# Kernel optimization log

Hardware: AMD Instinct MI355X
Metric: run time of the kernel (lower is better)

The kernel has to match this reference:

```python
import jax, jax.numpy as jnp
import numpy as np

C = 32          # d_model / channels
D_STATE = 32
D_CONV = 4
EXPAND = 2
D_INNER = EXPAND * C          # 64
DT_RANK = (C + 15) // 16      # ceil(32/16) = 2
EPS = 1e-5


def _conv2d(x, w, b):
    # x: (B,C,H,W), w: (O,I,3,3), stride 1, padding 1 (torch Conv2d)
    y = jax.lax.conv_general_dilated(
        x, w, window_strides=(1, 1), padding=[(1, 1), (1, 1)],
        dimension_numbers=("NCHW", "OIHW", "NCHW"))
    return y + b[None, :, None, None]


def _silu(x):
    return x * jax.nn.sigmoid(x)


def _mamba(xs, in_proj_w, conv1d_w, conv1d_b, x_proj_w, dt_proj_w, dt_proj_b,
           A_log, Dp, out_proj_w):
    # xs: (B, L, C)
    xz = xs @ in_proj_w.T                       # (B, L, 2*D_INNER)
    xm, z = jnp.split(xz, 2, axis=-1)           # each (B, L, D_INNER)

    # causal depthwise conv1d along L (torch: padding=d_conv-1 then [..., :L])
    xc = xm.transpose(0, 2, 1)                  # (B, D_INNER, L)
    xc = jax.lax.conv_general_dilated(
        xc, conv1d_w, window_strides=(1,), padding=[(D_CONV - 1, 0)],
        dimension_numbers=("NCH", "OIH", "NCH"),
        feature_group_count=D_INNER)
    xm = _silu((xc + conv1d_b[None, :, None]).transpose(0, 2, 1))  # (B,L,D_INNER)

    x_dbl = xm @ x_proj_w.T                     # (B, L, DT_RANK + 2*D_STATE)
    dt = x_dbl[..., :DT_RANK]
    Bm = x_dbl[..., DT_RANK:DT_RANK + D_STATE]  # (B, L, N)
    Cm = x_dbl[..., DT_RANK + D_STATE:]         # (B, L, N)

    delta = jax.nn.softplus(dt @ dt_proj_w.T + dt_proj_b)  # (B, L, D_INNER)
    A = -jnp.exp(A_log)                                     # (D_INNER, N)

    deltaA = jnp.exp(delta[..., None] * A)                           # (B,L,D,N)
    deltaBx = delta[..., None] * Bm[:, :, None, :] * xm[..., None]   # (B,L,D,N)

    def combine(c1, c2):
        a1, b1 = c1
        a2, b2 = c2
        return a1 * a2, a2 * b1 + b2

    # parallel linear recurrence h_t = deltaA_t * h_{t-1} + deltaBx_t
    _, hstate = jax.lax.associative_scan(combine, (deltaA, deltaBx), axis=1)

    y = jnp.einsum("bldn,bln->bld", hstate, Cm) + xm * Dp
    y = y * _silu(z)
    return y @ out_proj_w.T                     # (B, L, C)


def setup_inputs() -> dict:
    key = jax.random.key(0)
    ks = jax.random.split(key, 16)
    s = 0.02
    inp = {
        "x": jax.random.normal(ks[0], (4, C, 64, 64), dtype=jnp.float32),
        "conv1_w": jax.random.normal(ks[1], (2 * C, C, 3, 3), jnp.float32) * s,
        "conv1_b": jnp.zeros((2 * C,), jnp.float32),
        "conv2_w": jax.random.normal(ks[2], (C, 2 * C, 3, 3), jnp.float32) * s,
        "conv2_b": jnp.zeros((C,), jnp.float32),
        "ln_g": jnp.ones((C,), jnp.float32),
        "ln_b": jnp.zeros((C,), jnp.float32),
        "in_proj_w": jax.random.normal(ks[3], (2 * D_INNER, C), jnp.float32) * s,
        "conv1d_w": jax.random.normal(ks[4], (D_INNER, 1, D_CONV), jnp.float32) * 0.1,
        "conv1d_b": jnp.zeros((D_INNER,), jnp.float32),
        "x_proj_w": jax.random.normal(ks[5], (DT_RANK + 2 * D_STATE, D_INNER), jnp.float32) * s,
        "dt_proj_w": jax.random.normal(ks[6], (D_INNER, DT_RANK), jnp.float32) * 0.1,
        "dt_proj_b": jax.random.normal(ks[7], (D_INNER,), jnp.float32) * 0.1 - 4.0,
        "A_log": jnp.log(jnp.tile(jnp.arange(1, D_STATE + 1, dtype=jnp.float32), (D_INNER, 1))),
        "Dp": jnp.ones((D_INNER,), jnp.float32),
        "out_proj_w": jax.random.normal(ks[8], (C, D_INNER), jnp.float32) * s,
        "smooth_w": jax.random.normal(ks[9], (C, C, 3, 3), jnp.float32) * s,
        "smooth_b": jnp.zeros((C,), jnp.float32),
    }
    return inp


def reference(x, conv1_w, conv1_b, conv2_w, conv2_b, ln_g, ln_b,
              in_proj_w, conv1d_w, conv1d_b, x_proj_w, dt_proj_w, dt_proj_b,
              A_log, Dp, out_proj_w, smooth_w, smooth_b):
    b, c, h, w = x.shape
    # convb residual
    t = jax.nn.relu(_conv2d(x, conv1_w, conv1_b))
    x = _conv2d(t, conv2_w, conv2_b) + x
    # reshape (b,c,h,w) -> (b, h*w, c) row-major (faithful to torch .reshape)
    xs = x.reshape(b, -1, c)
    # LayerNorm over last dim
    mu = jnp.mean(xs, axis=-1, keepdims=True)
    var = jnp.mean(jnp.square(xs - mu), axis=-1, keepdims=True)
    xs = (xs - mu) * jax.lax.rsqrt(var + EPS) * ln_g + ln_b
    # Mamba block
    y = _mamba(xs, in_proj_w, conv1d_w, conv1d_b, x_proj_w, dt_proj_w,
               dt_proj_b, A_log, Dp, out_proj_w)
    y = y.transpose(0, 2, 1).reshape(b, c, h, w)
    return _conv2d(y, smooth_w, smooth_b)
```

## Files before the change

### kernel.cpp

```cpp
#include <hip/hip_runtime.h>
#include <math.h>

#define SEQL 4096
#define L2E 1.44269504088896340736f

#if defined(__has_builtin)
#if __has_builtin(__builtin_amdgcn_exp2f)
#define FAST_EXP2(x) __builtin_amdgcn_exp2f(x)
#endif
#endif
#ifndef FAST_EXP2
#define FAST_EXP2(x) exp2f(x)
#endif

__device__ __forceinline__ float sigmoid_f(float x){ return 1.0f/(1.0f+expf(-x)); }

template<int CI, int CO, int COG, bool RELU, bool RES>
__global__ __launch_bounds__(256) void conv3x3_k(const float* __restrict__ in,
    const float* __restrict__ wgt, const float* __restrict__ bias,
    const float* __restrict__ res, float* __restrict__ out)
{
  constexpr int CIT = CI/4;
  __shared__ float tin[4][2][6][72];
  __shared__ float red[3][4][COG][66];
  const int tid  = threadIdx.x;
  const int lane = tid & 63;
  const int ty   = tid >> 6;
  const int tyu  = __builtin_amdgcn_readfirstlane(ty);
  const int h0   = blockIdx.x * 4;
  const int co0  = blockIdx.y * COG;
  const int b    = blockIdx.z;

  if (lane < 24){
    int cl = lane / 12, rem = lane % 12, r = rem >> 1, side = rem & 1;
    tin[ty][cl][r][side ? 68 : 3] = 0.0f;
  }

  float acc[4][COG];
  #pragma unroll
  for (int rr=0;rr<4;++rr)
    #pragma unroll
    for (int u=0;u<COG;++u) acc[rr][u] = 0.0f;

  const int ci0 = tyu*CIT;
  for (int cig = ci0; cig < ci0 + CIT; cig += 2){
    #pragma unroll
    for (int k=0;k<3;++k){
      int idx4 = lane + (k<<6);
      int row  = idx4 >> 4;
      int cl = row/6, r = row - cl*6;
      int w4 = (idx4 & 15) << 2;
      int h  = h0 - 1 + r;
      float4 v = make_float4(0.f,0.f,0.f,0.f);
      if (h>=0 && h<64)
        v = *(const float4*)(in + ((size_t)(b*CI+cig+cl)*64 + h)*64 + w4);
      *(float4*)&tin[ty][cl][r][4+w4] = v;
    }
    #pragma unroll
    for (int cl=0; cl<2; ++cl){
      float rv[6][3];
      #pragma unroll
      for (int r=0;r<6;++r)
        #pragma unroll
        for (int c=0;c<3;++c)
          rv[r][c] = tin[ty][cl][r][3+lane+c];
      #pragma unroll
      for (int u=0;u<COG;++u){
        const float* wp = wgt + ((size_t)(co0+u)*CI + cig + cl)*9;
        #pragma unroll
        for (int rr=0;rr<4;++rr)
          #pragma unroll
          for (int j=0;j<3;++j){
            acc[rr][u] = fmaf(rv[rr+j][0], wp[3*j+0], acc[rr][u]);
            acc[rr][u] = fmaf(rv[rr+j][1], wp[3*j+1], acc[rr][u]);
            acc[rr][u] = fmaf(rv[rr+j][2], wp[3*j+2], acc[rr][u]);
          }
      }
    }
  }
  if (ty > 0){
    #pragma unroll
    for (int rr=0;rr<4;++rr)
      #pragma unroll
      for (int u=0;u<COG;++u) red[ty-1][rr][u][lane] = acc[rr][u];
  }
  __syncthreads();
  if (ty == 0){
    #pragma unroll
    for (int rr=0;rr<4;++rr)
      #pragma unroll
      for (int u=0;u<COG;++u){
        float s = acc[rr][u] + red[0][rr][u][lane] + red[1][rr][u][lane]
                + red[2][rr][u][lane] + bias[co0+u];
        size_t ob = ((size_t)(b*CO+co0+u)*64 + h0+rr)*64 + lane;
        if constexpr (RES)  s += res[ob];
        if constexpr (RELU) s = fmaxf(s, 0.0f);
        out[ob] = s;
      }
  }
}

__global__ __launch_bounds__(1024, 4) void mamba_in_k(const float* __restrict__ x2,
    const float* __restrict__ g, const float* __restrict__ be,
    const float* __restrict__ Wip, const float* __restrict__ cw,
    const float* __restrict__ cb, const float* __restrict__ Wxp,
    const float* __restrict__ Wdt, const float* __restrict__ bdt,
    const float* __restrict__ A_log,
    float* __restrict__ xm2, float* __restrict__ szb, float* __restrict__ dlt,
    float* __restrict__ Bm, float* __restrict__ Cm,
    float* __restrict__ cA, float* __restrict__ cH)
{
  __shared__ __align__(16) float xn[68][37];
  __shared__ __align__(16) float xm[64][68];
  __shared__ __align__(16) float xtT[64][68];
  __shared__ __align__(16) float xd[64][67];
  float (*xbT)[68] = reinterpret_cast<float(*)[68]>(&xn[0][0]);
  const int tid = threadIdx.x, lane = tid & 63, ty = tid >> 6;
  const int tyu = __builtin_amdgcn_readfirstlane(ty);
  const int bi = blockIdx.x >> 6;
  const int l0 = (blockIdx.x & 63) << 6;

  {
    const int row = tid >> 3, sub = tid & 7;
    if (row < 67){
      const int tok = l0 - 3 + row;
      const int c0 = sub << 2;
      if (tok >= 0){
        float4 f = *(const float4*)(x2 + (size_t)bi*131072 + (size_t)tok*32 + c0);
        float s = (f.x+f.y)+(f.z+f.w);
        s += __shfl_xor(s,1); s += __shfl_xor(s,2); s += __shfl_xor(s,4);
        const float mu = s * 0.03125f;
        float dx=f.x-mu, dy=f.y-mu, dz=f.z-mu, dw=f.w-mu;
        float q = (dx*dx+dy*dy)+(dz*dz+dw*dw);
        q += __shfl_xor(q,1); q += __shfl_xor(q,2); q += __shfl_xor(q,4);
        const float rstd = 1.0f/sqrtf(q*0.03125f + 1e-5f);
        float4 gv = *(const float4*)(g  + c0);
        float4 bv = *(const float4*)(be + c0);
        xn[row][c0+0] = dx*rstd*gv.x + bv.x;
        xn[row][c0+1] = dy*rstd*gv.y + bv.y;
        xn[row][c0+2] = dz*rstd*gv.z + bv.z;
        xn[row][c0+3] = dw*rstd*gv.w + bv.w;
      } else {
        xn[row][c0+0]=0.0f; xn[row][c0+1]=0.0f;
        xn[row][c0+2]=0.0f; xn[row][c0+3]=0.0f;
      }
    }
  }
  __syncthreads();

  if (ty < 8){
    const int d0 = tyu*8;
    float xvA[32];
    #pragma unroll
    for (int c=0;c<32;++c) xvA[c] = xn[lane][c];
    #pragma unroll
    for (int jj=0;jj<8;++jj){
      const float4* wr = (const float4*)(Wip + (d0+jj)*32);
      float a = 0.0f;
      #pragma unroll
      for (int c4=0;c4<8;++c4){
        float4 w = wr[c4];
        a = fmaf(xvA[c4*4+0], w.x, a);
        a = fmaf(xvA[c4*4+1], w.y, a);
        a = fmaf(xvA[c4*4+2], w.z, a);
        a = fmaf(xvA[c4*4+3], w.w, a);
      }
      xm[d0+jj][lane] = a;
    }
    if (lane < 3){
      float xvB[32];
      #pragma unroll
      for (int c=0;c<32;++c) xvB[c] = xn[64+lane][c];
      #pragma unroll
      for (int jj=0;jj<8;++jj){
        const float4* wr = (const float4*)(Wip + (d0+jj)*32);
        float a = 0.0f;
        #pragma unroll
        for (int c4=0;c4<8;++c4){
          float4 w = wr[c4];
          a = fmaf(xvB[c4*4+0], w.x, a);
          a = fmaf(xvB[c4*4+1], w.y, a);
          a = fmaf(xvB[c4*4+2], w.z, a);
          a = fmaf(xvB[c4*4+3], w.w, a);
        }
        xm[d0+jj][64+lane] = a;
      }
    }
  } else {
    const int d0z = (tyu-8)*8;
    float xvC[32];
    #pragma unroll
    for (int c=0;c<32;++c) xvC[c] = xn[lane+3][c];
    #pragma unroll
    for (int jj=0;jj<8;++jj){
      const float4* wr = (const float4*)(Wip + (64+d0z+jj)*32);
      float a = 0.0f;
      #pragma unroll
      for (int c4=0;c4<8;++c4){
        float4 w = wr[c4];
        a = fmaf(xvC[c4*4+0], w.x, a);
        a = fmaf(xvC[c4*4+1], w.y, a);
        a = fmaf(xvC[c4*4+2], w.z, a);
        a = fmaf(xvC[c4*4+3], w.w, a);
      }
      szb[((size_t)(bi*64+d0z+jj))*SEQL + l0 + lane] = a * sigmoid_f(a);
    }
  }
  __syncthreads();

  #pragma unroll
  for (int jj=0;jj<4;++jj){
    int d = tyu*4 + jj;
    float4 w = *(const float4*)(cw + d*4);
    float a = xm[d][lane]*w.x + xm[d][lane+1]*w.y
            + xm[d][lane+2]*w.z + xm[d][lane+3]*w.w + cb[d];
    float s = a * sigmoid_f(a);
    xtT[d][lane] = s;
    xm2[((size_t)(bi*64+d))*SEQL + l0 + lane] = s;
  }
  __syncthreads();

  {
    float xv[64];
    #pragma unroll
    for (int c=0;c<64;++c) xv[c] = xtT[c][lane];
    for (int j=tyu; j<66; j+=16){
      const float4* wr = (const float4*)(Wxp + j*64);
      float a = 0.0f;
      #pragma unroll
      for (int c4=0;c4<16;++c4){
        float4 w = wr[c4];
        a = fmaf(xv[c4*4+0], w.x, a);
        a = fmaf(xv[c4*4+1], w.y, a);
        a = fmaf(xv[c4*4+2], w.z, a);
        a = fmaf(xv[c4*4+3], w.w, a);
      }
      xd[lane][j] = a;
    }
  }
  __syncthreads();

  {
    float dt0 = xd[lane][0], dt1 = xd[lane][1];
    #pragma unroll
    for (int k=0;k<4;++k){
      int d2 = tyu*4 + k;
      float2 wd = *(const float2*)(Wdt + d2*2);
      float v = dt0*wd.x + dt1*wd.y + bdt[d2];
      float sp = fmaxf(v,0.0f) + log1pf(expf(-fabsf(v)));
      dlt[((size_t)(bi*64+d2))*SEQL + l0 + lane] = sp;
      xm[d2][lane] = sp;
    }
    const int which = tyu >> 3, gq = tyu & 7;
    float* dst = which ? Cm : Bm;
    size_t base = ((size_t)bi*SEQL + l0 + lane)*32 + gq*4;
    const int s2 = 2 + which*32;
    float4 f0;
    f0.x = xd[lane][s2+gq+ 0]; f0.y = xd[lane][s2+gq+ 8];
    f0.z = xd[lane][s2+gq+16]; f0.w = xd[lane][s2+gq+24];
    *(float4*)(dst + base) = f0;
    if (!which){
      xbT[gq     ][lane] = f0.x;
      xbT[gq +  8][lane] = f0.y;
      xbT[gq + 16][lane] = f0.z;
      xbT[gq + 24][lane] = f0.w;
    }
  }
  __syncthreads();

  {
    const int d  = tid >> 4;
    const int gg = tid & 15;
    const int chunk = blockIdx.x & 63;
    const int bd = bi*64 + d;
    float Av0 = -expf(A_log[d*32 + gg     ]) * L2E;
    float Av1 = -expf(A_log[d*32 + gg + 16]) * L2E;
    float h0=0.0f, h1=0.0f, aP0=1.0f, aP1=1.0f;
    #pragma unroll 2
    for (int t0=0;t0<64;t0+=4){
      float4 dl4 = *(const float4*)&xm [d    ][t0];
      float4 xs4 = *(const float4*)&xtT[d    ][t0];
      float4 b04 = *(const float4*)&xbT[gg   ][t0];
      float4 b14 = *(const float4*)&xbT[gg+16][t0];
      #pragma unroll
      for (int k=0;k<4;++k){
        float dlv = (k==0)? dl4.x : (k==1)? dl4.y : (k==2)? dl4.z : dl4.w;
        float xsv = (k==0)? xs4.x : (k==1)? xs4.y : (k==2)? xs4.z : xs4.w;
        float bv0 = (k==0)? b04.x : (k==1)? b04.y : (k==2)? b04.z : b04.w;
        float bv1 = (k==0)? b14.x : (k==1)? b14.y : (k==2)? b14.z : b14.w;
        float m  = dlv * xsv;
        float a0 = FAST_EXP2(dlv*Av0);
        float a1 = FAST_EXP2(dlv*Av1);
        h0 = fmaf(a0, h0, m*bv0);  aP0 *= a0;
        h1 = fmaf(a1, h1, m*bv1);  aP1 *= a1;
      }
    }
    size_t base = ((size_t)bd*64 + chunk)*32;
    cA[base + gg] = aP0; cA[base + gg + 16] = aP1;
    cH[base + gg] = h0;  cH[base + gg + 16] = h1;
  }
}

__global__ __launch_bounds__(1024, 4) void mamba_out_k(const float* __restrict__ dlt,
    const float* __restrict__ xssm, const float* __restrict__ szb,
    const float* __restrict__ Bm, const float* __restrict__ Cm,
    const float* __restrict__ A_log, const float* __restrict__ Dp,
    const float* __restrict__ cA, const float* __restrict__ cHs,
    const float* __restrict__ Wout, float* __restrict__ ym)
{
  __shared__ __align__(16) float dl32[64][36];
  __shared__ __align__(16) float xs32[64][36];
  __shared__ __align__(16) float z32 [64][36];
  __shared__ __align__(16) float B32 [32][36];
  __shared__ __align__(16) float ct32[32][34];
  __shared__ __align__(16) float ysT [64][68];
  const int tid = threadIdx.x, lane = tid & 63, ty = tid >> 6;
  const int tyu = __builtin_amdgcn_readfirstlane(ty);
  const int bi = blockIdx.x >> 6;
  const int chunk = blockIdx.x & 63;
  const int l0 = chunk << 6;

  const int d = tid >> 4, gg = tid & 15;
  const int bd = bi*64 + d;
  const float Av0 = -expf(A_log[d*32 + gg     ]) * L2E;
  const float Av1 = -expf(A_log[d*32 + gg + 16]) * L2E;
  const float Dv  = Dp[d];

  float h0 = 0.0f, h1 = 0.0f;
  {
    const float* pa = cA  + (size_t)bd*64*32;
    const float* ph = cHs + (size_t)bd*64*32;
    #pragma unroll 4
    for (int c = 0; c < chunk; ++c){
      float a0 = pa[c*32 + gg     ], q0 = ph[c*32 + gg     ];
      float a1 = pa[c*32 + gg + 16], q1 = ph[c*32 + gg + 16];
      h0 = fmaf(a0, h0, q0);
      h1 = fmaf(a1, h1, q1);
    }
  }

  #pragma unroll
  for (int s = 0; s < 2; ++s){
    const int t0 = s << 5;
    if (tid < 512){
      int dd = tid >> 3, f = (tid & 7) << 2;
      *(float4*)&dl32[dd][f] = *(const float4*)(dlt + (size_t)(bi*64+dd)*SEQL + l0 + t0 + f);
      *(float4*)&z32 [dd][f] = *(const float4*)(szb + (size_t)(bi*64+dd)*SEQL + l0 + t0 + f);
    } else {
      int u = tid - 512;
      int dd = u >> 3, f = (u & 7) << 2;
      *(float4*)&xs32[dd][f] = *(const float4*)(xssm + (size_t)(bi*64+dd)*SEQL + l0 + t0 + f);
      if (u < 256){
        int tok = u >> 3, q = u & 7;
        float4 fb = *(const float4*)(Bm + ((size_t)(bi*SEQL) + l0 + t0 + tok)*32 + q*4);
        B32[q     ][tok] = fb.x;
        B32[q +  8][tok] = fb.y;
        B32[q + 16][tok] = fb.z;
        B32[q + 24][tok] = fb.w;
      } else {
        int v = u - 256;
        int tok = v >> 3, q = v & 7;
        float4 fc = *(const float4*)(Cm + ((size_t)(bi*SEQL) + l0 + t0 + tok)*32 + q*4);
        ct32[tok][q     ] = fc.x;
        ct32[tok][q +  8] = fc.y;
        ct32[tok][q + 16] = fc.z;
        ct32[tok][q + 24] = fc.w;
      }
    }
    __syncthreads();

    #pragma unroll 4
    for (int t = 0; t < 32; ++t){
      float dlv = dl32[d][t];
      float xsv = xs32[d][t];
      float m   = dlv * xsv;
      float bv0 = B32[gg   ][t];
      float bv1 = B32[gg+16][t];
      float a0 = FAST_EXP2(dlv*Av0);
      float a1 = FAST_EXP2(dlv*Av1);
      h0 = fmaf(a0, h0, m*bv0);
      h1 = fmaf(a1, h1, m*bv1);
      float part = fmaf(h1, ct32[t][gg+16], h0*ct32[t][gg]);
      part += __shfl_xor(part,1); part += __shfl_xor(part,2);
      part += __shfl_xor(part,4); part += __shfl_xor(part,8);
      if (gg == 0)
        ysT[d][t0 + t] = fmaf(xsv, Dv, part) * z32[d][t];
    }
    __syncthreads();
  }

  {
    const float4* w0 = (const float4*)(Wout + tyu*64);
    const float4* w1 = (const float4*)(Wout + (tyu+16)*64);
    float a0 = 0.0f, a1 = 0.0f;
    #pragma unroll
    for (int c4 = 0; c4 < 16; ++c4){
      float4 wa = w0[c4], wb = w1[c4];
      float y0 = ysT[c4*4+0][lane];
      float y1 = ysT[c4*4+1][lane];
      float y2 = ysT[c4*4+2][lane];
      float y3 = ysT[c4*4+3][lane];
      a0 = fmaf(y3, wa.w, fmaf(y2, wa.z, fmaf(y1, wa.y, fmaf(y0, wa.x, a0))));
      a1 = fmaf(y3, wb.w, fmaf(y2, wb.z, fmaf(y1, wb.y, fmaf(y0, wb.x, a1))));
    }
    ym[(size_t)(bi*32 + tyu     )*SEQL + l0 + lane] = a0;
    ym[(size_t)(bi*32 + tyu + 16)*SEQL + l0 + lane] = a1;
  }
}

extern "C" void kernel_launch(void* const* d_in, const int* in_sizes, int n_in,
                              void* d_out, int out_size, void* d_ws, size_t ws_size,
                              hipStream_t stream) {
  const float* x        = (const float*)d_in[0];
  const float* conv1_w  = (const float*)d_in[1];
  const float* conv1_b  = (const float*)d_in[2];
  const float* conv2_w  = (const float*)d_in[3];
  const float* conv2_b  = (const float*)d_in[4];
  const float* ln_g     = (const float*)d_in[5];
  const float* ln_b     = (const float*)d_in[6];
  const float* in_proj_w= (const float*)d_in[7];
  const float* conv1d_w = (const float*)d_in[8];
  const float* conv1d_b = (const float*)d_in[9];
  const float* x_proj_w = (const float*)d_in[10];
  const float* dt_proj_w= (const float*)d_in[11];
  const float* dt_proj_b= (const float*)d_in[12];
  const float* A_log    = (const float*)d_in[13];
  const float* Dp       = (const float*)d_in[14];
  const float* out_proj_w=(const float*)d_in[15];
  const float* smooth_w = (const float*)d_in[16];
  const float* smooth_b = (const float*)d_in[17];
  float* out = (float*)d_out;

  float* ws = (float*)d_ws;
  float* t      = ws;
  float* x2     = t      + 1048576;
  float* xm2    = x2     + 524288;
  float* szb    = xm2    + 1048576;
  float* dlt    = szb    + 1048576;
  float* Bmat   = dlt    + 1048576;
  float* Cmat   = Bmat   + 524288;
  float* ym     = Cmat   + 524288;
  float* cA     = t;
  float* cH     = t + 524288;

  conv3x3_k<32,64,4,true ,false><<<dim3(16,16,4), 256, 0, stream>>>(x,  conv1_w, conv1_b, nullptr, t);
  conv3x3_k<64,32,4,false,true ><<<dim3(16,8,4), 256, 0, stream>>>(t,  conv2_w, conv2_b, x,       x2);
  mamba_in_k  <<<256, 1024, 0, stream>>>(x2, ln_g, ln_b, in_proj_w, conv1d_w, conv1d_b,
                                         x_proj_w, dt_proj_w, dt_proj_b, A_log,
                                         xm2, szb, dlt, Bmat, Cmat, cA, cH);
  mamba_out_k <<<256, 1024, 0, stream>>>(dlt, xm2, szb, Bmat, Cmat, A_log, Dp,
                                         cA, cH, out_proj_w, ym);
  conv3x3_k<32,32,4,false,false><<<dim3(16,8,4), 256, 0, stream>>>(ym, smooth_w, smooth_b, nullptr, out);
}
```

Baseline: 193.4 us.

## Split conv3x3 output channels across waves instead of input channels

The 3x3 conv kernel used to give each wave a slice of input channels and then reduce partial sums through shared memory. Now each wave owns its own output channels and the whole block shares a staged tile of 8 input channels, so the cross-wave reduction and its buffer go away. The price is a block-wide sync per input-channel stage and fewer output channels per wave (1-2 instead of 4), which lowers input reuse per loaded row. Grid sizes and per-conv templates change to match.

```diff
diff --git a/kernel.cpp b/kernel.cpp
--- a/kernel.cpp
+++ b/kernel.cpp
@@ -15,58 +15,57 @@
 
 __device__ __forceinline__ float sigmoid_f(float x){ return 1.0f/(1.0f+expf(-x)); }
 
-template<int CI, int CO, int COG, bool RELU, bool RES>
+template<int CI, int CO, int COW, bool RELU, bool RES>
 __global__ __launch_bounds__(256) void conv3x3_k(const float* __restrict__ in,
     const float* __restrict__ wgt, const float* __restrict__ bias,
     const float* __restrict__ res, float* __restrict__ out)
 {
-  constexpr int CIT = CI/4;
-  __shared__ float tin[4][2][6][72];
-  __shared__ float red[3][4][COG][66];
+  constexpr int CIS = 8;
+  constexpr int NST = CI / CIS;
+  __shared__ __align__(16) float tin[CIS][6][72];
   const int tid  = threadIdx.x;
   const int lane = tid & 63;
   const int ty   = tid >> 6;
   const int tyu  = __builtin_amdgcn_readfirstlane(ty);
   const int h0   = blockIdx.x * 4;
-  const int co0  = blockIdx.y * COG;
+  const int co0  = blockIdx.y * (4*COW) + tyu*COW;
   const int b    = blockIdx.z;
 
-  if (lane < 24){
-    int cl = lane / 12, rem = lane % 12, r = rem >> 1, side = rem & 1;
-    tin[ty][cl][r][side ? 68 : 3] = 0.0f;
-  }
-
-  float acc[4][COG];
+  float acc[4][COW];
   #pragma unroll
   for (int rr=0;rr<4;++rr)
     #pragma unroll
-    for (int u=0;u<COG;++u) acc[rr][u] = 0.0f;
-
-  const int ci0 = tyu*CIT;
-  for (int cig = ci0; cig < ci0 + CIT; cig += 2){
+    for (int u=0;u<COW;++u) acc[rr][u] = 0.0f;
+
+  for (int st=0; st<NST; ++st){
+    const int cig = st*CIS;
+    if (st) __syncthreads();
     #pragma unroll
     for (int k=0;k<3;++k){
-      int idx4 = lane + (k<<6);
-      int row  = idx4 >> 4;
-      int cl = row/6, r = row - cl*6;
-      int w4 = (idx4 & 15) << 2;
-      int h  = h0 - 1 + r;
+      int flat = tid + (k<<8);
+      int pair = flat >> 4;
+      int ci = pair / 6, row = pair - ci*6;
+      int w4 = (flat & 15) << 2;
+      int h  = h0 - 1 + row;
       float4 v = make_float4(0.f,0.f,0.f,0.f);
       if (h>=0 && h<64)
-        v = *(const float4*)(in + ((size_t)(b*CI+cig+cl)*64 + h)*64 + w4);
-      *(float4*)&tin[ty][cl][r][4+w4] = v;
-    }
-    #pragma unroll
-    for (int cl=0; cl<2; ++cl){
+        v = *(const float4*)(in + ((size_t)(b*CI+cig+ci)*64 + h)*64 + w4);
+      *(float4*)&tin[ci][row][4+w4] = v;
+      if (w4 == 0)  tin[ci][row][3]  = 0.0f;
+      if (w4 == 60) tin[ci][row][68] = 0.0f;
+    }
+    __syncthreads();
+    #pragma unroll
+    for (int ci=0; ci<CIS; ++ci){
       float rv[6][3];
       #pragma unroll
       for (int r=0;r<6;++r)
         #pragma unroll
         for (int c=0;c<3;++c)
-          rv[r][c] = tin[ty][cl][r][3+lane+c];
-      #pragma unroll
-      for (int u=0;u<COG;++u){
-        const float* wp = wgt + ((size_t)(co0+u)*CI + cig + cl)*9;
+          rv[r][c] = tin[ci][r][3+lane+c];
+      #pragma unroll
+      for (int u=0;u<COW;++u){
+        const float* wp = wgt + ((size_t)(co0+u)*CI + cig + ci)*9;
         #pragma unroll
         for (int rr=0;rr<4;++rr)
           #pragma unroll
@@ -78,25 +77,18 @@
       }
     }
   }
-  if (ty > 0){
-    #pragma unroll
-    for (int rr=0;rr<4;++rr)
-      #pragma unroll
-      for (int u=0;u<COG;++u) red[ty-1][rr][u][lane] = acc[rr][u];
-  }
-  __syncthreads();
-  if (ty == 0){
-    #pragma unroll
-    for (int rr=0;rr<4;++rr)
-      #pragma unroll
-      for (int u=0;u<COG;++u){
-        float s = acc[rr][u] + red[0][rr][u][lane] + red[1][rr][u][lane]
-                + red[2][rr][u][lane] + bias[co0+u];
-        size_t ob = ((size_t)(b*CO+co0+u)*64 + h0+rr)*64 + lane;
-        if constexpr (RES)  s += res[ob];
-        if constexpr (RELU) s = fmaxf(s, 0.0f);
-        out[ob] = s;
-      }
+
+  #pragma unroll
+  for (int u=0;u<COW;++u){
+    const float bv = bias[co0+u];
+    #pragma unroll
+    for (int rr=0;rr<4;++rr){
+      float s = acc[rr][u] + bv;
+      size_t ob = ((size_t)(b*CO+co0+u)*64 + h0+rr)*64 + lane;
+      if constexpr (RES)  s += res[ob];
+      if constexpr (RELU) s = fmaxf(s, 0.0f);
+      out[ob] = s;
+    }
   }
 }
 
@@ -443,12 +435,12 @@
   float* cA     = t;
   float* cH     = t + 524288;
 
-  conv3x3_k<32,64,4,true ,false><<<dim3(16,16,4), 256, 0, stream>>>(x,  conv1_w, conv1_b, nullptr, t);
-  conv3x3_k<64,32,4,false,true ><<<dim3(16,8,4), 256, 0, stream>>>(t,  conv2_w, conv2_b, x,       x2);
+  conv3x3_k<32,64,2,true ,false><<<dim3(16,8,4), 256, 0, stream>>>(x,  conv1_w, conv1_b, nullptr, t);
+  conv3x3_k<64,32,1,false,true ><<<dim3(16,8,4), 256, 0, stream>>>(t,  conv2_w, conv2_b, x,       x2);
   mamba_in_k  <<<256, 1024, 0, stream>>>(x2, ln_g, ln_b, in_proj_w, conv1d_w, conv1d_b,
                                          x_proj_w, dt_proj_w, dt_proj_b, A_log,
                                          xm2, szb, dlt, Bmat, Cmat, cA, cH);
   mamba_out_k <<<256, 1024, 0, stream>>>(dlt, xm2, szb, Bmat, Cmat, A_log, Dp,
                                          cA, cH, out_proj_w, ym);
-  conv3x3_k<32,32,4,false,false><<<dim3(16,8,4), 256, 0, stream>>>(ym, smooth_w, smooth_b, nullptr, out);
+  conv3x3_k<32,32,1,false,false><<<dim3(16,8,4), 256, 0, stream>>>(ym, smooth_w, smooth_b, nullptr, out);
 }
```

Measured after the change: 206.0 us. 1.07x slower.
